# Optimization experiments

Measured on AMD Instinct MI355X. Metric: run time of the kernel, lower is better.

## Reference

```python
import jax, jax.numpy as jnp
import numpy as np

D_IN = 1024
D_OUT = 1024
BATCH = 4
SEQ = 2048


def setup_inputs() -> dict:
    key = jax.random.key(0)
    kx, kq, kk, kv = jax.random.split(key, 4)
    # nn.Linear default init: U(-1/sqrt(d_in), 1/sqrt(d_in)); exact dist irrelevant for a reference
    bound = 1.0 / np.sqrt(D_IN)
    x = jax.random.normal(kx, (BATCH, SEQ, D_IN), dtype=jnp.float32)
    W_query = jax.random.uniform(kq, (D_IN, D_OUT), dtype=jnp.float32, minval=-bound, maxval=bound)
    W_key = jax.random.uniform(kk, (D_IN, D_OUT), dtype=jnp.float32, minval=-bound, maxval=bound)
    W_value = jax.random.uniform(kv, (D_IN, D_OUT), dtype=jnp.float32, minval=-bound, maxval=bound)
    return {"x": x, "W_query": W_query, "W_key": W_key, "W_value": W_value}


def reference(x, W_query, W_key, W_value):
    # x: [b, s, d_in]; projections (qkv_bias=False)
    q = jnp.einsum("bsd,df->bsf", x, W_query)  # [b, s, d_out]
    k = jnp.einsum("bsd,df->bsf", x, W_key)
    v = jnp.einsum("bsd,df->bsf", x, W_value)

    scale = 1.0 / jnp.sqrt(jnp.asarray(k.shape[-1], dtype=x.dtype))
    scores = jnp.einsum("bqf,bkf->bqk", q, k) * scale  # [b, s, s]

    s = x.shape[1]
    causal = jnp.tril(jnp.ones((s, s), dtype=bool))  # True where allowed
    scores = jnp.where(causal[None, :, :], scores, -jnp.inf)

    weights = jax.nn.softmax(scores, axis=-1)
    # dropout_ratio=0.0 -> identity
    return jnp.einsum("bqk,bkf->bqf", weights, v)  # [b, s, d_out]
```

## Files before the change

kernel.cpp:

```cpp
#include <hip/hip_runtime.h>


typedef __bf16 bf16x8 __attribute__((ext_vector_type(8)));
typedef float f32x4 __attribute__((ext_vector_type(4)));

__device__ __forceinline__ unsigned short f2bf(float f) {
  unsigned int u = __builtin_bit_cast(unsigned int, f);
  u += 0x7FFFu + ((u >> 16) & 1u);
  return (unsigned short)(u >> 16);
}
__device__ __forceinline__ float bf2f(unsigned short h) {
  unsigned int u = ((unsigned int)h) << 16;
  return __builtin_bit_cast(float, u);
}

#define GLDS16(g, l)                                                                   \
  __builtin_amdgcn_global_load_lds((const __attribute__((address_space(1))) void*)(g), \
                                   (__attribute__((address_space(3))) void*)(l), 16, 0, 0)

__global__ __launch_bounds__(256) void k_cvt(const float* __restrict__ in,
                                             unsigned short* __restrict__ out, long n) {
  long i = ((long)blockIdx.x * 256 + threadIdx.x) * 8;
  if (i >= n) return;
  float4 a = *(const float4*)(in + i);
  float4 b = *(const float4*)(in + i + 4);
  uint4 o;
  o.x = (unsigned)f2bf(a.x) | ((unsigned)f2bf(a.y) << 16);
  o.y = (unsigned)f2bf(a.z) | ((unsigned)f2bf(a.w) << 16);
  o.z = (unsigned)f2bf(b.x) | ((unsigned)f2bf(b.y) << 16);
  o.w = (unsigned)f2bf(b.z) | ((unsigned)f2bf(b.w) << 16);
  *(uint4*)(out + i) = o;
}

__global__ void k_trans_w(const float* __restrict__ W0, const float* __restrict__ W1,
                          const float* __restrict__ W2, unsigned short* __restrict__ Wt, int D) {
  const float* W = blockIdx.z == 0 ? W0 : (blockIdx.z == 1 ? W1 : W2);
  unsigned short* out = Wt + (long)blockIdx.z * D * D;
  __shared__ float tile[32][33];
  int tx = threadIdx.x, ty = threadIdx.y;
  int bx = blockIdx.x * 32, by = blockIdx.y * 32;
#pragma unroll
  for (int j = 0; j < 4; ++j) tile[ty + j * 8][tx] = W[(long)(by + ty + j * 8) * D + bx + tx];
  __syncthreads();
#pragma unroll
  for (int j = 0; j < 4; ++j)
    out[(long)(bx + ty + j * 8) * D + by + tx] = f2bf(tile[tx][ty + j * 8]);
}

template <typename CT>
__global__ __launch_bounds__(512, 2) void k_gemm256(const unsigned short* __restrict__ A,
                                                    const unsigned short* __restrict__ B,
                                                    CT* __restrict__ C, int nx, int ny, int N,
                                                    int K, long sA, long sB, long sC,
                                                    float alpha) {
  const unsigned bid = blockIdx.x;
  const unsigned cpx = gridDim.x >> 3;
  const unsigned logical = (bid & 7) * cpx + (bid >> 3);
  const int per_z = nx * ny;
  const int z = (int)(logical / per_z);
  const int rem = (int)(logical - (unsigned)z * per_z);
  const int by = rem / nx;
  const int bx = rem - by * nx;
  const int m0 = by * 256, n0 = bx * 256;
  A += (long)z * sA;
  B += (long)z * sB;
  C += (long)z * sC;

  __shared__ char lds[131072];

  const int t = threadIdx.x;
  const int l = t & 63;
  const int w = t >> 6;
  const int wm = w >> 2;
  const int wn = w & 3;

  const int srow = t >> 3;
  const int sch = (t & 7) ^ (srow & 7);
  const int soff = t * 16;

#define STG(mat, bf, hf, kt)                                                              \
  do {                                                                                    \
    const unsigned short* g =                                                             \
        ((mat) ? B + (long)(n0 + (hf)*128 + srow) * K : A + (long)(m0 + (hf)*128 + srow) * K) + \
        (long)(kt)*64 + sch * 8;                                                          \
    char* d = lds + (mat)*65536 + (bf)*32768 + (hf)*16384 + soff;                         \
    GLDS16(g, d);                                                                         \
    GLDS16(g + (long)64 * K, d + 8192);                                                   \
  } while (0)

  const int lx = l & 15;
  const int kx0 = ((l >> 4) ^ (l & 7)) * 16;
  const int kx1 = ((4 + (l >> 4)) ^ (l & 7)) * 16;
  char* const aB = lds + wm * 16384 + lx * 128;
  char* const bB = lds + 65536 + (wn >> 1) * 16384 + ((wn & 1) * 64 + lx) * 128;

  bf16x8 av[4][2], bv0[2][2], bv1[2][2];
  f32x4 acc[8][4];
#pragma unroll
  for (int i = 0; i < 8; ++i)
#pragma unroll
    for (int jn = 0; jn < 4; ++jn) acc[i][jn] = f32x4{0.f, 0.f, 0.f, 0.f};

#define RDA(bf, mh)                                                     \
  do {                                                                  \
    _Pragma("unroll") for (int m4 = 0; m4 < 4; ++m4) {                  \
      char* p = aB + (bf)*32768 + ((mh)*64 + m4 * 16) * 128;            \
      av[m4][0] = *(const bf16x8*)(p + kx0);                            \
      av[m4][1] = *(const bf16x8*)(p + kx1);                            \
    }                                                                   \
  } while (0)
#define RDB(dst, bf, nh)                                                \
  do {                                                                  \
    _Pragma("unroll") for (int n2 = 0; n2 < 2; ++n2) {                  \
      char* p = bB + (bf)*32768 + (((nh)*2 + n2) * 16) * 128;           \
      dst[n2][0] = *(const bf16x8*)(p + kx0);                           \
      dst[n2][1] = *(const bf16x8*)(p + kx1);                           \
    }                                                                   \
  } while (0)
#define MFM(bv, mh, nh)                                                                    \
  do {                                                                                     \
    __builtin_amdgcn_s_setprio(1);                                                         \
    _Pragma("unroll") for (int m4 = 0; m4 < 4; ++m4) _Pragma("unroll") for (int n2 = 0;    \
                                                                            n2 < 2; ++n2) { \
      acc[(mh)*4 + m4][(nh)*2 + n2] = __builtin_amdgcn_mfma_f32_16x16x32_bf16(             \
          av[m4][0], bv[n2][0], acc[(mh)*4 + m4][(nh)*2 + n2], 0, 0, 0);                   \
      acc[(mh)*4 + m4][(nh)*2 + n2] = __builtin_amdgcn_mfma_f32_16x16x32_bf16(             \
          av[m4][1], bv[n2][1], acc[(mh)*4 + m4][(nh)*2 + n2], 0, 0, 0);                   \
    }                                                                                      \
    __builtin_amdgcn_s_setprio(0);                                                         \
  } while (0)
#define BAR __builtin_amdgcn_s_barrier()
#define VMC(n) asm volatile("s_waitcnt vmcnt(" #n ")" ::: "memory")

  const int KT = K >> 6;
  const int NIT = KT >> 1;

  STG(0, 0, 0, 0); STG(0, 0, 1, 0); STG(1, 0, 0, 0); STG(1, 0, 1, 0);
  STG(1, 1, 0, 1); STG(1, 1, 1, 1); STG(0, 1, 0, 1);
  VMC(6);
  BAR;

  for (int j = 0; j < NIT; ++j) {
    const bool full = (j < NIT - 1);
    RDA(0, 0); RDB(bv0, 0, 0);
    STG(0, 1, 1, 2 * j + 1);
    BAR; MFM(bv0, 0, 0); BAR;
    RDB(bv1, 0, 1);
    BAR; MFM(bv1, 0, 1); BAR;
    RDA(0, 1);
    if (full) STG(1, 0, 0, 2 * j + 2);
    BAR; MFM(bv1, 1, 1); BAR;
    if (full) {
      STG(0, 0, 0, 2 * j + 2); STG(1, 0, 1, 2 * j + 2);
      VMC(6);
    } else {
      VMC(0);
    }
    BAR; MFM(bv0, 1, 0); BAR;
    RDA(1, 0); RDB(bv0, 1, 0);
    if (full) STG(0, 0, 1, 2 * j + 2);
    BAR; MFM(bv0, 0, 0); BAR;
    RDB(bv1, 1, 1);
    BAR; MFM(bv1, 0, 1); BAR;
    RDA(1, 1);
    if (full) STG(1, 1, 0, 2 * j + 3);
    BAR; MFM(bv1, 1, 1); BAR;
    if (full) {
      STG(1, 1, 1, 2 * j + 3); STG(0, 1, 0, 2 * j + 3);
      VMC(6);
    }
    BAR; MFM(bv0, 1, 0); BAR;
  }

  const int rb = m0 + wm * 128 + (l >> 4) * 4;
  const int cb = n0 + wn * 64 + (l & 15);
#pragma unroll
  for (int m = 0; m < 8; ++m)
#pragma unroll
    for (int n = 0; n < 4; ++n)
#pragma unroll
      for (int i = 0; i < 4; ++i) {
        float v = acc[m][n][i] * alpha;
        long off = (long)(rb + m * 16 + i) * N + (cb + n * 16);
        if constexpr (sizeof(CT) == 2)
          C[off] = f2bf(v);
        else
          C[off] = v;
      }
#undef STG
#undef RDA
#undef RDB
#undef MFM
#undef BAR
#undef VMC
}

template <typename CT>
__global__ __launch_bounds__(256) void k_gemm_bt(const unsigned short* __restrict__ A,
                                                 const unsigned short* __restrict__ B,
                                                 CT* __restrict__ C, int nx, int ny, int N, int K,
                                                 long sA, long sB, long sC, float alpha) {
  const unsigned bid = blockIdx.x;
  const unsigned cpx = gridDim.x >> 3;
  const unsigned logical = (bid & 7) * cpx + (bid >> 3);
  const int per_z = nx * ny;
  const int z = (int)(logical / per_z);
  const int r = (int)(logical - (unsigned)z * per_z);
  const int by = r / nx;
  const int bx = r - by * nx;
  const int m0 = by * 128;
  const int n0 = bx * 128;
  A += (long)z * sA;
  B += (long)z * sB;
  C += (long)z * sC;

  __shared__ unsigned short As[128 * 64];
  __shared__ unsigned short Bs[128 * 64];
  char* const AsB = (char*)As;
  char* const BsB = (char*)Bs;

  const int t = threadIdx.x;
  const int l = t & 63;
  const int w = t >> 6;
  const int wr = (w >> 1) * 64;
  const int wc = (w & 1) * 64;

  const int srow = t >> 3;
  const int sch = (t & 7) ^ (srow & 7);
  const unsigned short* Ag = A + (long)(m0 + srow) * K + sch * 8;
  const unsigned short* Bg = B + (long)(n0 + srow) * K + sch * 8;
  const int soff = t * 16;

  const int ar = wr + (l & 15);
  const int brr = wc + (l & 15);
  const int kc = l >> 4;

  f32x4 acc[4][4];
#pragma unroll
  for (int i = 0; i < 4; ++i)
#pragma unroll
    for (int j = 0; j < 4; ++j) acc[i][j] = f32x4{0.f, 0.f, 0.f, 0.f};

  const int KT = K >> 6;
  for (int kt = 0; kt < KT; ++kt) {
    const long ko = (long)kt * 64;
#pragma unroll
    for (int i = 0; i < 4; ++i) GLDS16(Ag + (long)i * 32 * K + ko, AsB + i * 4096 + soff);
#pragma unroll
    for (int i = 0; i < 4; ++i) GLDS16(Bg + (long)i * 32 * K + ko, BsB + i * 4096 + soff);
    __syncthreads();
#pragma unroll
    for (int kk = 0; kk < 2; ++kk) {
      bf16x8 av[4], bv[4];
#pragma unroll
      for (int m = 0; m < 4; ++m) {
        int rr = ar + m * 16;
        int c = (kk * 4 + kc) ^ (rr & 7);
        av[m] = *(const bf16x8*)(AsB + rr * 128 + c * 16);
      }
#pragma unroll
      for (int n = 0; n < 4; ++n) {
        int rr = brr + n * 16;
        int c = (kk * 4 + kc) ^ (rr & 7);
        bv[n] = *(const bf16x8*)(BsB + rr * 128 + c * 16);
      }
#pragma unroll
      for (int m = 0; m < 4; ++m)
#pragma unroll
        for (int n = 0; n < 4; ++n)
          acc[m][n] = __builtin_amdgcn_mfma_f32_16x16x32_bf16(av[m], bv[n], acc[m][n], 0, 0, 0);
    }
    __syncthreads();
  }

  const int rb = m0 + wr + (l >> 4) * 4;
  const int cb = n0 + wc + (l & 15);
#pragma unroll
  for (int m = 0; m < 4; ++m)
#pragma unroll
    for (int n = 0; n < 4; ++n)
#pragma unroll
      for (int i = 0; i < 4; ++i) {
        float v = acc[m][n][i] * alpha;
        long off = (long)(rb + m * 16 + i) * N + (cb + n * 16);
        if constexpr (sizeof(CT) == 2)
          C[off] = f2bf(v);
        else
          C[off] = v;
      }
}

template <typename CT, int MODE>
__global__ __launch_bounds__(256) void k_gemm_bt64(const unsigned short* __restrict__ A,
                                                   const unsigned short* __restrict__ B,
                                                   CT* __restrict__ C, int N, int K, long sA,
                                                   long sB, long sC, float alpha) {
  const unsigned bid = blockIdx.x;
  const unsigned cpx = gridDim.x >> 3;
  const unsigned logical = (bid & 7) * cpx + (bid >> 3);
  int z, by, bx;
  if constexpr (MODE == 0) {
    const int per_z = 272;
    z = (int)(logical / per_z);
    int r = (int)(logical - (unsigned)z * per_z);
    int b = (int)((sqrtf(4.f * (float)r + 1.f) - 1.f) * 0.5f);
    while ((b + 1) * (b + 2) <= r) ++b;
    while (b * (b + 1) > r) --b;
    by = b;
    bx = r - b * (b + 1);
  } else {
    const int nx = N >> 6;
    const int per_z = 8 * nx;
    z = (int)(logical / per_z);
    int r = (int)(logical - (unsigned)z * per_z);
    by = r / nx;
    bx = r - by * nx;
  }
  A += (long)z * sA;
  B += (long)z * sB;
  C += (long)z * sC;

  __shared__ unsigned short As[128 * 64];
  __shared__ unsigned short Bs[64 * 64];
  char* const AsB = (char*)As;
  char* const BsB = (char*)Bs;

  const int t = threadIdx.x;
  const int l = t & 63;
  const int w = t >> 6;
  const int wr = (w >> 1) * 64;
  const int wc = (w & 1) * 32;

  const int srow = t >> 3;
  const int sch = (t & 7) ^ (srow & 7);
  const int soff = t * 16;

  const int ar = wr + (l & 15);
  const int brr = wc + (l & 15);
  const int kc = l >> 4;

  const int n0 = bx * 64;
  const unsigned short* Bg = B + (long)(n0 + srow) * K + sch * 8;

  const int nseg = (MODE == 1) ? 2 : 1;
  for (int seg = 0; seg < nseg; ++seg) {
    const int row = (MODE == 1) ? (seg ? (15 - by) : by) : by;
    const int m0 = row * 128;
    const int KT = (MODE == 1) ? ((m0 + 128) >> 6) : (K >> 6);
    const unsigned short* Ag = A + (long)(m0 + srow) * K + sch * 8;

    f32x4 acc[4][2];
#pragma unroll
    for (int i = 0; i < 4; ++i)
#pragma unroll
      for (int j = 0; j < 2; ++j) acc[i][j] = f32x4{0.f, 0.f, 0.f, 0.f};

    for (int kt = 0; kt < KT; ++kt) {
      const long ko = (long)kt * 64;
#pragma unroll
      for (int i = 0; i < 4; ++i) GLDS16(Ag + (long)i * 32 * K + ko, AsB + i * 4096 + soff);
#pragma unroll
      for (int i = 0; i < 2; ++i) GLDS16(Bg + (long)i * 32 * K + ko, BsB + i * 4096 + soff);
      __syncthreads();
#pragma unroll
      for (int kk = 0; kk < 2; ++kk) {
        bf16x8 av[4], bv[2];
#pragma unroll
        for (int m = 0; m < 4; ++m) {
          int rr = ar + m * 16;
          int c = (kk * 4 + kc) ^ (rr & 7);
          av[m] = *(const bf16x8*)(AsB + rr * 128 + c * 16);
        }
#pragma unroll
        for (int n = 0; n < 2; ++n) {
          int rr = brr + n * 16;
          int c = (kk * 4 + kc) ^ (rr & 7);
          bv[n] = *(const bf16x8*)(BsB + rr * 128 + c * 16);
        }
#pragma unroll
        for (int m = 0; m < 4; ++m)
#pragma unroll
          for (int n = 0; n < 2; ++n)
            acc[m][n] = __builtin_amdgcn_mfma_f32_16x16x32_bf16(av[m], bv[n], acc[m][n], 0, 0, 0);
      }
      __syncthreads();
    }

    const int rb = m0 + wr + (l >> 4) * 4;
    const int cb = n0 + wc + (l & 15);
#pragma unroll
    for (int m = 0; m < 4; ++m)
#pragma unroll
      for (int n = 0; n < 2; ++n)
#pragma unroll
        for (int i = 0; i < 4; ++i) {
          float v = acc[m][n][i] * alpha;
          long off = (long)(rb + m * 16 + i) * N + (cb + n * 16);
          if constexpr (sizeof(CT) == 2)
            C[off] = f2bf(v);
          else
            C[off] = v;
        }
  }
}

__global__ __launch_bounds__(256) void k_softmax(unsigned short* __restrict__ P, int S) {
  const int t = threadIdx.x;
  const int wv = t >> 6, l = t & 63;
  const int q = blockIdx.x * 4 + wv;
  unsigned short* row = P + ((long)blockIdx.y * S + q) * S;
  const int nch = (q >> 9) + 1;

  uint4 raw[4];
  float v[32];
#pragma unroll
  for (int j = 0; j < 4; ++j)
    if (j < nch) raw[j] = ((const uint4*)row)[j * 64 + l];
#pragma unroll
  for (int j = 0; j < 4; ++j) {
    if (j < nch) {
      unsigned int rw[4] = {raw[j].x, raw[j].y, raw[j].z, raw[j].w};
#pragma unroll
      for (int e = 0; e < 8; ++e)
        v[j * 8 + e] = bf2f((unsigned short)((rw[e >> 1] >> ((e & 1) * 16)) & 0xFFFF));
    }
  }

  float mx = -3.0e38f;
#pragma unroll
  for (int j = 0; j < 4; ++j)
    if (j < nch) {
#pragma unroll
      for (int e = 0; e < 8; ++e) {
        int col = j * 512 + l * 8 + e;
        if (col <= q) mx = fmaxf(mx, v[j * 8 + e]);
      }
    }
#pragma unroll
  for (int o = 32; o >= 1; o >>= 1) mx = fmaxf(mx, __shfl_xor(mx, o, 64));

  float s = 0.f;
#pragma unroll
  for (int j = 0; j < 4; ++j)
    if (j < nch) {
#pragma unroll
      for (int e = 0; e < 8; ++e) {
        int col = j * 512 + l * 8 + e;
        float ev = (col <= q) ? __expf(v[j * 8 + e] - mx) : 0.f;
        v[j * 8 + e] = ev;
        s += ev;
      }
    }
#pragma unroll
  for (int o = 32; o >= 1; o >>= 1) s += __shfl_xor(s, o, 64);
  const float inv = 1.f / s;

#pragma unroll
  for (int j = 0; j < 4; ++j)
    if (j < nch) {
      uint4 ow;
      unsigned int o2[4];
#pragma unroll
      for (int jj = 0; jj < 4; ++jj)
        o2[jj] = (unsigned)f2bf(v[j * 8 + 2 * jj] * inv) |
                 ((unsigned)f2bf(v[j * 8 + 2 * jj + 1] * inv) << 16);
      ow.x = o2[0]; ow.y = o2[1]; ow.z = o2[2]; ow.w = o2[3];
      ((uint4*)row)[j * 64 + l] = ow;
    }
}

extern "C" void kernel_launch(void* const* d_in, const int* in_sizes, int n_in, void* d_out,
                              int out_size, void* d_ws, size_t ws_size, hipStream_t stream) {
  const int B = 4, S = 2048, D = 1024;
  const long MS = (long)B * S;

  const float* x = (const float*)d_in[0];
  const float* Wq = (const float*)d_in[1];
  const float* Wk = (const float*)d_in[2];
  const float* Wv = (const float*)d_in[3];
  float* out = (float*)d_out;

  unsigned short* xb = (unsigned short*)d_ws;
  unsigned short* Wt = xb + MS * D;
  unsigned short* Qb = Wt + 3L * D * D;
  unsigned short* Kb = Qb + MS * D;
  unsigned short* Vt = Kb + MS * D;
  unsigned short* P  = Vt + MS * D;
  (void)ws_size;

  long n = MS * D;
  k_cvt<<<dim3((unsigned)(n / 8 / 256)), 256, 0, stream>>>(x, xb, n);
  k_trans_w<<<dim3(32, 32, 3), dim3(32, 8), 0, stream>>>(Wq, Wk, Wv, Wt, D);
  k_gemm256<unsigned short><<<256, 512, 0, stream>>>(
      xb, Wt, Qb, D / 256, (int)(MS / 256), D, D,
      0L, (long)D * D, MS * D, 1.0f);
  k_gemm_bt<unsigned short><<<512, 256, 0, stream>>>(
      Wt + 2L * D * D, xb, Vt, S / 128, D / 128, S, D,
      0L, (long)S * D, (long)D * S, 1.0f);
  k_gemm_bt64<unsigned short, 0><<<1088, 256, 0, stream>>>(
      Qb, Kb, P, S, D,
      (long)S * D, (long)S * D, (long)S * S, 0.03125f);
  k_softmax<<<dim3(S / 4, B), 256, 0, stream>>>(P, S);
  k_gemm_bt64<float, 1><<<512, 256, 0, stream>>>(
      P, Vt, out, D, S,
      (long)S * S, (long)D * S, (long)S * D, 1.0f);
}
```

Baseline: 145.3 us.

## Double-buffer LDS in P·V GEMM and merge prep kernels into one launch

Adds a DBUF template option to the 64-wide GEMM. When it is on, the kernel prefetches the next K tile into a second LDS buffer with global_load_lds while the MFMAs run on the current one, synchronising with explicit vmcnt waits and s_barrier. It is enabled only for the P·V GEMM, which doubles that kernel's LDS use and may lower occupancy. The fp32-to-bf16 conversion of x and the weight transpose are also merged into a single launch to save one kernel launch.

```diff
diff --git a/kernel.cpp b/kernel.cpp
--- a/kernel.cpp
+++ b/kernel.cpp
@@ -18,27 +18,37 @@
   __builtin_amdgcn_global_load_lds((const __attribute__((address_space(1))) void*)(g), \
                                    (__attribute__((address_space(3))) void*)(l), 16, 0, 0)
 
-__global__ __launch_bounds__(256) void k_cvt(const float* __restrict__ in,
-                                             unsigned short* __restrict__ out, long n) {
-  long i = ((long)blockIdx.x * 256 + threadIdx.x) * 8;
-  if (i >= n) return;
-  float4 a = *(const float4*)(in + i);
-  float4 b = *(const float4*)(in + i + 4);
-  uint4 o;
-  o.x = (unsigned)f2bf(a.x) | ((unsigned)f2bf(a.y) << 16);
-  o.y = (unsigned)f2bf(a.z) | ((unsigned)f2bf(a.w) << 16);
-  o.z = (unsigned)f2bf(b.x) | ((unsigned)f2bf(b.y) << 16);
-  o.w = (unsigned)f2bf(b.z) | ((unsigned)f2bf(b.w) << 16);
-  *(uint4*)(out + i) = o;
-}
-
-__global__ void k_trans_w(const float* __restrict__ W0, const float* __restrict__ W1,
-                          const float* __restrict__ W2, unsigned short* __restrict__ Wt, int D) {
-  const float* W = blockIdx.z == 0 ? W0 : (blockIdx.z == 1 ? W1 : W2);
-  unsigned short* out = Wt + (long)blockIdx.z * D * D;
+__global__ __launch_bounds__(256) void k_prep(const float* __restrict__ x,
+                                              unsigned short* __restrict__ xb,
+                                              const float* __restrict__ W0,
+                                              const float* __restrict__ W1,
+                                              const float* __restrict__ W2,
+                                              unsigned short* __restrict__ Wt, long n, int ncvt,
+                                              int D) {
+  const int b = blockIdx.x;
+  const int t = threadIdx.x;
+  if (b < ncvt) {
+    long i = ((long)b * 256 + t) * 8;
+    if (i >= n) return;
+    float4 a = *(const float4*)(x + i);
+    float4 c = *(const float4*)(x + i + 4);
+    uint4 o;
+    o.x = (unsigned)f2bf(a.x) | ((unsigned)f2bf(a.y) << 16);
+    o.y = (unsigned)f2bf(a.z) | ((unsigned)f2bf(a.w) << 16);
+    o.z = (unsigned)f2bf(c.x) | ((unsigned)f2bf(c.y) << 16);
+    o.w = (unsigned)f2bf(c.z) | ((unsigned)f2bf(c.w) << 16);
+    *(uint4*)(xb + i) = o;
+    return;
+  }
+  const int id = b - ncvt;
+  const int nt = (D / 32) * (D / 32);
+  const int z = id / nt;
+  const int rem = id - z * nt;
+  const int by = (rem >> 5) * 32, bx = (rem & 31) * 32;
+  const float* W = z == 0 ? W0 : (z == 1 ? W1 : W2);
+  unsigned short* out = Wt + (long)z * D * D;
   __shared__ float tile[32][33];
-  int tx = threadIdx.x, ty = threadIdx.y;
-  int bx = blockIdx.x * 32, by = blockIdx.y * 32;
+  const int tx = t & 31, ty = t >> 5;
 #pragma unroll
   for (int j = 0; j < 4; ++j) tile[ty + j * 8][tx] = W[(long)(by + ty + j * 8) * D + bx + tx];
   __syncthreads();
@@ -290,7 +300,7 @@
       }
 }
 
-template <typename CT, int MODE>
+template <typename CT, int MODE, int DBUF>
 __global__ __launch_bounds__(256) void k_gemm_bt64(const unsigned short* __restrict__ A,
                                                    const unsigned short* __restrict__ B,
                                                    CT* __restrict__ C, int N, int K, long sA,
@@ -320,8 +330,8 @@
   B += (long)z * sB;
   C += (long)z * sC;
 
-  __shared__ unsigned short As[128 * 64];
-  __shared__ unsigned short Bs[64 * 64];
+  __shared__ unsigned short As[(1 + DBUF) * 128 * 64];
+  __shared__ unsigned short Bs[(1 + DBUF) * 64 * 64];
   char* const AsB = (char*)As;
   char* const BsB = (char*)Bs;
 
@@ -341,6 +351,35 @@
 
   const int n0 = bx * 64;
   const unsigned short* Bg = B + (long)(n0 + srow) * K + sch * 8;
+
+#define STG64(Agp, kt, bf)                                                           \
+  do {                                                                               \
+    const long ko = (long)(kt)*64;                                                   \
+    _Pragma("unroll") for (int i = 0; i < 4; ++i)                                    \
+        GLDS16((Agp) + (long)i * 32 * K + ko, AsB + (bf)*16384 + i * 4096 + soff);   \
+    _Pragma("unroll") for (int i = 0; i < 2; ++i)                                    \
+        GLDS16(Bg + (long)i * 32 * K + ko, BsB + (bf)*8192 + i * 4096 + soff);       \
+  } while (0)
+
+#define CMP64(bf)                                                                    \
+  do {                                                                               \
+    _Pragma("unroll") for (int kk = 0; kk < 2; ++kk) {                               \
+      bf16x8 av[4], bv[2];                                                           \
+      _Pragma("unroll") for (int m = 0; m < 4; ++m) {                                \
+        int rr = ar + m * 16;                                                        \
+        int c = (kk * 4 + kc) ^ (rr & 7);                                            \
+        av[m] = *(const bf16x8*)(AsB + (bf)*16384 + rr * 128 + c * 16);              \
+      }                                                                              \
+      _Pragma("unroll") for (int n = 0; n < 2; ++n) {                                \
+        int rr = brr + n * 16;                                                       \
+        int c = (kk * 4 + kc) ^ (rr & 7);                                            \
+        bv[n] = *(const bf16x8*)(BsB + (bf)*8192 + rr * 128 + c * 16);               \
+      }                                                                              \
+      _Pragma("unroll") for (int m = 0; m < 4; ++m) _Pragma("unroll") for (int n = 0; \
+                                                                          n < 2; ++n) \
+          acc[m][n] = __builtin_amdgcn_mfma_f32_16x16x32_bf16(av[m], bv[n], acc[m][n], 0, 0, 0); \
+    }                                                                                \
+  } while (0)
 
   const int nseg = (MODE == 1) ? 2 : 1;
   for (int seg = 0; seg < nseg; ++seg) {
@@ -355,35 +394,26 @@
 #pragma unroll
       for (int j = 0; j < 2; ++j) acc[i][j] = f32x4{0.f, 0.f, 0.f, 0.f};
 
-    for (int kt = 0; kt < KT; ++kt) {
-      const long ko = (long)kt * 64;
-#pragma unroll
-      for (int i = 0; i < 4; ++i) GLDS16(Ag + (long)i * 32 * K + ko, AsB + i * 4096 + soff);
-#pragma unroll
-      for (int i = 0; i < 2; ++i) GLDS16(Bg + (long)i * 32 * K + ko, BsB + i * 4096 + soff);
-      __syncthreads();
-#pragma unroll
-      for (int kk = 0; kk < 2; ++kk) {
-        bf16x8 av[4], bv[2];
-#pragma unroll
-        for (int m = 0; m < 4; ++m) {
-          int rr = ar + m * 16;
-          int c = (kk * 4 + kc) ^ (rr & 7);
-          av[m] = *(const bf16x8*)(AsB + rr * 128 + c * 16);
+    if constexpr (DBUF) {
+      STG64(Ag, 0, 0);
+      for (int kt = 0; kt < KT; ++kt) {
+        if (kt + 1 < KT) {
+          STG64(Ag, kt + 1, (kt + 1) & 1);
+          asm volatile("s_waitcnt vmcnt(6)" ::: "memory");
+        } else {
+          asm volatile("s_waitcnt vmcnt(0)" ::: "memory");
         }
-#pragma unroll
-        for (int n = 0; n < 2; ++n) {
-          int rr = brr + n * 16;
-          int c = (kk * 4 + kc) ^ (rr & 7);
-          bv[n] = *(const bf16x8*)(BsB + rr * 128 + c * 16);
-        }
-#pragma unroll
-        for (int m = 0; m < 4; ++m)
-#pragma unroll
-          for (int n = 0; n < 2; ++n)
-            acc[m][n] = __builtin_amdgcn_mfma_f32_16x16x32_bf16(av[m], bv[n], acc[m][n], 0, 0, 0);
-      }
-      __syncthreads();
+        __builtin_amdgcn_s_barrier();
+        CMP64(kt & 1);
+        __builtin_amdgcn_s_barrier();
+      }
+    } else {
+      for (int kt = 0; kt < KT; ++kt) {
+        STG64(Ag, kt, 0);
+        __syncthreads();
+        CMP64(0);
+        __syncthreads();
+      }
     }
 
     const int rb = m0 + wr + (l >> 4) * 4;
@@ -402,6 +432,8 @@
             C[off] = v;
         }
   }
+#undef STG64
+#undef CMP64
 }
 
 __global__ __launch_bounds__(256) void k_softmax(unsigned short* __restrict__ P, int S) {
@@ -489,19 +521,20 @@
   (void)ws_size;
 
   long n = MS * D;
-  k_cvt<<<dim3((unsigned)(n / 8 / 256)), 256, 0, stream>>>(x, xb, n);
-  k_trans_w<<<dim3(32, 32, 3), dim3(32, 8), 0, stream>>>(Wq, Wk, Wv, Wt, D);
+  const int ncvt = (int)(n / 8 / 256);
+  const int ntrw = 3 * (D / 32) * (D / 32);
+  k_prep<<<ncvt + ntrw, 256, 0, stream>>>(x, xb, Wq, Wk, Wv, Wt, n, ncvt, D);
   k_gemm256<unsigned short><<<256, 512, 0, stream>>>(
       xb, Wt, Qb, D / 256, (int)(MS / 256), D, D,
       0L, (long)D * D, MS * D, 1.0f);
   k_gemm_bt<unsigned short><<<512, 256, 0, stream>>>(
       Wt + 2L * D * D, xb, Vt, S / 128, D / 128, S, D,
       0L, (long)S * D, (long)D * S, 1.0f);
-  k_gemm_bt64<unsigned short, 0><<<1088, 256, 0, stream>>>(
+  k_gemm_bt64<unsigned short, 0, 0><<<1088, 256, 0, stream>>>(
       Qb, Kb, P, S, D,
       (long)S * D, (long)S * D, (long)S * S, 0.03125f);
   k_softmax<<<dim3(S / 4, B), 256, 0, stream>>>(P, S);
-  k_gemm_bt64<float, 1><<<512, 256, 0, stream>>>(
+  k_gemm_bt64<float, 1, 1><<<512, 256, 0, stream>>>(
       P, Vt, out, D, S,
       (long)S * S, (long)D * S, (long)S * D, 1.0f);
 }
```

New measurement: 141.9 us. 2.4% less time.
